# Kernel tuning notes

Hardware: AMD Instinct MI355X
Metric: run time of the kernel (lower is better)

## Reference

```python
import jax, jax.numpy as jnp
import numpy as np

EPS = 1e-5
MIN_NORM = 1e-10

def _norm(x):
    return jnp.sqrt(jnp.clip(jnp.sum(x * x, axis=-1, keepdims=True), MIN_NORM, None))

def _proj(x):
    # clip points to the open unit Poincare ball
    n = _norm(x)
    max_n = 1.0 - EPS
    return jnp.where(n > max_n, x * (max_n / n), x)

def _artanh(x):
    return jnp.arctanh(jnp.clip(x, -1.0 + EPS, 1.0 - EPS))

def mob_add(u, v):
    uv = jnp.sum(u * v, axis=-1, keepdims=True)
    u2 = jnp.sum(u * u, axis=-1, keepdims=True)
    v2 = jnp.sum(v * v, axis=-1, keepdims=True)
    num = (1.0 + 2.0 * uv + v2) * u + (1.0 - u2) * v
    den = 1.0 + 2.0 * uv + u2 * v2
    return _proj(num / jnp.maximum(den, MIN_NORM))

def mob_mat_mul(M, x):
    # M: [Din, Dout], x: [B, Din] on the ball. Ganea Mobius matvec.
    x = _proj(x)
    Mx = x @ M
    x_n = _norm(x)
    Mx_n = _norm(Mx)
    return _proj(jnp.tanh(Mx_n / x_n * _artanh(x_n)) * (Mx / Mx_n))

def log_map_zero(y):
    n = _norm(y)
    return _artanh(n) * y / n

def exp_map_zero(v):
    n = _norm(v)
    return _proj(jnp.tanh(n) * v / n)

def mob_pointwise_prod(x, u):
    # coordinate-wise scale of hyperbolic x by gate u, in the tangent space at 0
    return exp_map_zero(log_map_zero(x) * u)

def _transition(W, h, U, x, b):
    Wh = mob_mat_mul(W, h)
    Ux = mob_mat_mul(U, x)
    return mob_add(mob_add(Wh, Ux), b)

def setup_inputs() -> dict:
    B, I, H = 2048, 1024, 1024
    Din, Dh = 2 * I, 2 * H
    k = (1.0 / H) ** 0.5
    key = jax.random.key(0)
    ks = jax.random.split(key, 8)
    return {
        "hyp_x": jax.random.normal(ks[0], (B, Din), jnp.float32) * 0.01,
        "hidden": jax.random.normal(ks[1], (B, Dh), jnp.float32) * 0.01,
        "w_z": jax.random.uniform(ks[2], (Dh, Dh), jnp.float32, -k, k),
        "w_r": jax.random.uniform(ks[3], (Dh, Dh), jnp.float32, -k, k),
        "w_h": jax.random.uniform(ks[4], (Dh, Dh), jnp.float32, -k, k),
        "u_z": jax.random.uniform(ks[5], (Din, Dh), jnp.float32, -k, k),
        "u_r": jax.random.uniform(ks[6], (Din, Dh), jnp.float32, -k, k),
        "b_z": jnp.zeros((Dh,), jnp.float32),
        "b_r": jnp.zeros((Dh,), jnp.float32),
        "b_h": jnp.zeros((Dh,), jnp.float32),
    }

def reference(hyp_x, hidden, w_z, w_r, w_h, u_z, u_r, b_z, b_r, b_h):
    hyp_x = _proj(hyp_x)
    hidden = _proj(hidden)
    z = jax.nn.sigmoid(log_map_zero(_transition(w_z, hidden, u_z, hyp_x, b_z)))
    r = jax.nn.sigmoid(log_map_zero(_transition(w_r, hidden, u_r, hyp_x, b_r)))
    r_point_h = mob_pointwise_prod(hidden, r)
    # NOTE: original source uses u_r (not u_h) here; replicated faithfully.
    h_tilde = _transition(w_h, r_point_h, u_r, hyp_x, b_h)
    minus_h_oplus_htilde = mob_add(-hidden, h_tilde)
    new_h = mob_add(hidden, mob_pointwise_prod(minus_h_oplus_htilde, z))
    return new_h
```

## Files before the change

### kernel.cpp

```cpp
#include <hip/hip_runtime.h>
#include <hip/hip_bf16.h>
#include <math.h>

#define EPS 1e-5f
#define MAXN (1.0f - EPS)
#define MINN 1e-10f

constexpr int D = 2048;

typedef unsigned short u16;
typedef __bf16 bf16x8 __attribute__((ext_vector_type(8)));
typedef float floatx4 __attribute__((ext_vector_type(4)));


__device__ __forceinline__ u16 f2bf(float f) {
    union { float f; unsigned u; } v; v.f = f;
    unsigned r = v.u + 0x7FFFu + ((v.u >> 16) & 1u);
    return (u16)(r >> 16);
}

__device__ __forceinline__ float bf2f(u16 b) {
    union { unsigned u; float f; } v; v.u = ((unsigned)b) << 16; return v.f;
}

__device__ __forceinline__ void load_bf8(const u16* p, float* d) {
    uint4 r = *(const uint4*)p;
    unsigned w[4] = {r.x, r.y, r.z, r.w};
    #pragma unroll
    for (int i = 0; i < 4; ++i) {
        d[2 * i]     = bf2f((u16)(w[i] & 0xFFFFu));
        d[2 * i + 1] = bf2f((u16)(w[i] >> 16));
    }
}

__device__ __forceinline__ void store_bf8(u16* p, const float* s) {
    u16 pk[8];
    #pragma unroll
    for (int i = 0; i < 8; ++i) pk[i] = f2bf(s[i]);
    *(uint4*)p = *(const uint4*)pk;
}

__device__ __forceinline__ void load_f8(const float* p, float* d) {
    *(float4*)(d)     = *(const float4*)(p);
    *(float4*)(d + 4) = *(const float4*)(p + 4);
}

__device__ __forceinline__ void store_f8(float* p, const float* s) {
    *(float4*)(p)     = *(const float4*)(s);
    *(float4*)(p + 4) = *(const float4*)(s + 4);
}

__device__ __forceinline__ float artanh_(float x) {
    x = fminf(fmaxf(x, -1.0f + EPS), 1.0f - EPS);
    return 0.5f * logf((1.0f + x) / (1.0f - x));
}

__device__ __forceinline__ float sigmoid_(float x) {
    return 1.0f / (1.0f + expf(-x));
}

__device__ __forceinline__ void gl_lds16(const u16* g, u16* l) {
    __builtin_amdgcn_global_load_lds(
        (const __attribute__((address_space(1))) unsigned int*)g,
        (__attribute__((address_space(3))) unsigned int*)l, 16, 0, 0);
}

template<int N>
__device__ __forceinline__ void block_sums(float* v, float* sbuf) {
    #pragma unroll
    for (int n = 0; n < N; ++n)
        #pragma unroll
        for (int off = 32; off >= 1; off >>= 1) v[n] += __shfl_xor(v[n], off, 64);
    int w = threadIdx.x >> 6;
    __syncthreads();
    if ((threadIdx.x & 63) == 0) {
        #pragma unroll
        for (int n = 0; n < N; ++n) sbuf[w * N + n] = v[n];
    }
    __syncthreads();
    #pragma unroll
    for (int n = 0; n < N; ++n)
        v[n] = sbuf[n] + sbuf[N + n] + sbuf[2 * N + n] + sbuf[3 * N + n];
}

__device__ __forceinline__ void mmm_finish(float sum2, float g, float* coef, float* onorm) {
    float mxn = sqrtf(fmaxf(sum2, MINN));
    float tt  = tanhf(mxn * g);
    float on  = fminf(tt, MAXN);
    *coef = on / mxn;
    *onorm = on;
}

__device__ __forceinline__ float mob_apply(float* u, const float* v,
                                           float u2, float v2, float duv) {
    float cu  = 1.f + 2.f * duv + v2;
    float cv  = 1.f - u2;
    float den = fmaxf(1.f + 2.f * duv + u2 * v2, MINN);
    float s2  = cu * cu * u2 + 2.f * cu * cv * duv + cv * cv * v2;
    float n   = sqrtf(fmaxf(s2 / (den * den), MINN));
    float sc  = ((n > MAXN) ? MAXN / n : 1.f) / den;
    #pragma unroll
    for (int i = 0; i < 8; ++i) u[i] = sc * (cu * u[i] + cv * v[i]);
    return fminf(n, MAXN);
}

__device__ __forceinline__ void trans_tile(const float* W, u16* Wt,
                                           int n0, int k0, float* tile) {
    int t = threadIdx.x;
    int lr = t >> 4, lc = (t & 15) * 4;
    #pragma unroll
    for (int p = 0; p < 4; ++p) {
        int r = lr + p * 16;
        float4 v = *(const float4*)(W + (size_t)(k0 + r) * D + n0 + lc);
        tile[r * 65 + lc + 0] = v.x;
        tile[r * 65 + lc + 1] = v.y;
        tile[r * 65 + lc + 2] = v.z;
        tile[r * 65 + lc + 3] = v.w;
    }
    __syncthreads();
    int wn = t >> 3, ws = (t & 7) * 8;
    #pragma unroll
    for (int p = 0; p < 2; ++p) {
        int n = wn + p * 32;
        u16 pk[8];
        #pragma unroll
        for (int j = 0; j < 8; ++j) pk[j] = f2bf(tile[(ws + j) * 65 + n]);
        *(uint4*)(Wt + (size_t)(n0 + n) * D + k0 + ws) = *(uint4*)pk;
    }
}


struct PrepBatch {
    const float* W[5]; u16* Wt[5];
    const float* hx; const float* h;
    u16* hx_bf; u16* h_bf;
    float* g_x; float* g_h;
};

__global__ __launch_bounds__(256) void wtrans_prep(PrepBatch pb) {
    __shared__ float tile[64 * 65];
    int t = threadIdx.x;

    if (blockIdx.z != 4) {
        int wi = (blockIdx.z == 5) ? 4 : blockIdx.z;
        trans_tile(pb.W[wi], pb.Wt[wi],
                   blockIdx.x * 64, blockIdx.y * 64, tile);
    } else {
        int bid = blockIdx.y * (D / 64) + blockIdx.x;
        for (int rr = 0; rr < 2; ++rr) {
            int b = bid * 2 + rr;
            size_t off = (size_t)b * D + t * 8;
            float xv[8], hv[8];
            load_f8(pb.hx + off, xv);
            load_f8(pb.h + off, hv);
            float s[2] = {0.f, 0.f};
            #pragma unroll
            for (int i = 0; i < 8; ++i) { s[0] += xv[i] * xv[i]; s[1] += hv[i] * hv[i]; }
            block_sums<2>(s, tile);

            float nx = sqrtf(fmaxf(s[0], MINN));
            float scx = (nx > MAXN) ? MAXN / nx : 1.0f;
            float nh = sqrtf(fmaxf(s[1], MINN));
            float sch = (nh > MAXN) ? MAXN / nh : 1.0f;
            #pragma unroll
            for (int i = 0; i < 8; ++i) { xv[i] *= scx; hv[i] *= sch; }
            store_bf8(pb.hx_bf + off, xv);
            store_bf8(pb.h_bf + off, hv);
            if (t == 0) {
                float xn = fminf(nx, MAXN), hn = fminf(nh, MAXN);
                pb.g_x[b] = artanh_(xn) / xn;
                pb.g_h[b] = artanh_(hn) / hn;
            }
        }
    }
}


#define PHASE_MID() do { \
    __builtin_amdgcn_s_barrier(); \
    __builtin_amdgcn_s_setprio(1); } while (0)

#define PHASE_END() do { \
    __builtin_amdgcn_s_setprio(0); \
    __builtin_amdgcn_s_barrier(); } while (0)

template<int KLEN, int NJ>
__device__ __forceinline__ void gemm256_body(const u16* __restrict__ A,
                                             const u16* __restrict__ W,
                                             u16* __restrict__ C, int koff,
                                             u16* As, u16* Ws) {
    constexpr int T  = KLEN / 64;
    constexpr int BN = NJ * 64;
    constexpr int AU = 8192;
    constexpr int BU = BN * 32;

    int t0 = threadIdx.x;
    int wave = t0 >> 6, lane = t0 & 63, l16 = lane & 15, quad = lane >> 4;
    int wr = wave >> 2, wc = wave & 3;
    int brow = blockIdx.y * 256, bcol = blockIdx.x * BN;

    int srow = t0 >> 2;
    int sseg = (t0 & 3) ^ ((srow >> 1) & 3);
    const u16* srcA = A + (size_t)(brow + srow) * D + koff + sseg * 8;
    const u16* srcB = W + (size_t)(bcol + srow) * D + koff + sseg * 8;
    u16* ldsA = As + wave * 512;
    u16* ldsB = Ws + wave * 512;

    auto stageA = [&](int buf, int kh, int tile) {
        const u16* s = srcA + tile * 64 + kh * 32;
        u16* d = ldsA + (buf * 2 + kh) * AU;
        gl_lds16(s, d);
        gl_lds16(s + (size_t)128 * D, d + 4096);
    };
    auto stageB = [&](int buf, int kh, int tile) {
        const u16* s = srcB + tile * 64 + kh * 32;
        u16* d = ldsB + (buf * 2 + kh) * BU;
        gl_lds16(s, d);
        if constexpr (NJ == 4) gl_lds16(s + (size_t)128 * D, d + 4096);
    };

    const u16* aF = As + (wr * 128 + l16) * 32 + ((quad ^ ((l16 >> 1) & 3)) * 8);
    const u16* bF = Ws + (wc * (NJ * 16) + l16) * 32 + ((quad ^ ((l16 >> 1) & 3)) * 8);

    floatx4 acc[8][NJ];
    #pragma unroll
    for (int i = 0; i < 8; ++i)
        #pragma unroll
        for (int j = 0; j < NJ; ++j)
            #pragma unroll
            for (int e = 0; e < 4; ++e) acc[i][j][e] = 0.f;

    stageA(0, 0, 0); stageB(0, 0, 0);
    stageA(0, 1, 0); stageB(0, 1, 0);
    stageA(1, 0, 1); stageB(1, 0, 1);
    if constexpr (NJ == 4) asm volatile("s_waitcnt vmcnt(4)" ::: "memory");
    else                   asm volatile("s_waitcnt vmcnt(3)" ::: "memory");
    __builtin_amdgcn_s_barrier();

    #pragma unroll 2
    for (int tt = 0; tt < T; ++tt) {
        int bsel = tt & 1, bno = bsel ^ 1;
        const u16* aT = aF + bsel * (2 * AU);
        const u16* bT = bF + bsel * (2 * BU);
        bool st1 = (tt + 1) < T, st2 = (tt + 2) < T;

        if constexpr (NJ == 4) {
            bf16x8 bfr[4], afr[4];
            #pragma unroll
            for (int j = 0; j < 4; ++j) bfr[j] = *(const bf16x8*)(bT + j * 512);
            #pragma unroll
            for (int i = 0; i < 4; ++i) afr[i] = *(const bf16x8*)(aT + i * 512);
            if (st1) stageA(bno, 1, tt + 1);
            PHASE_MID();
            #pragma unroll
            for (int i = 0; i < 4; ++i)
                #pragma unroll
                for (int j = 0; j < 4; ++j)
                    acc[i][j] = __builtin_amdgcn_mfma_f32_16x16x32_bf16(afr[i], bfr[j], acc[i][j], 0, 0, 0);
            PHASE_END();
            #pragma unroll
            for (int i = 0; i < 4; ++i) afr[i] = *(const bf16x8*)(aT + (4 + i) * 512);
            if (st1) stageB(bno, 1, tt + 1);
            PHASE_MID();
            #pragma unroll
            for (int i = 0; i < 4; ++i)
                #pragma unroll
                for (int j = 0; j < 4; ++j)
                    acc[4 + i][j] = __builtin_amdgcn_mfma_f32_16x16x32_bf16(afr[i], bfr[j], acc[4 + i][j], 0, 0, 0);
            PHASE_END();
            #pragma unroll
            for (int j = 0; j < 4; ++j) bfr[j] = *(const bf16x8*)(bT + BU + j * 512);
            #pragma unroll
            for (int i = 0; i < 4; ++i) afr[i] = *(const bf16x8*)(aT + AU + i * 512);
            if (st2) stageA(bsel, 0, tt + 2);
            PHASE_MID();
            #pragma unroll
            for (int i = 0; i < 4; ++i)
                #pragma unroll
                for (int j = 0; j < 4; ++j)
                    acc[i][j] = __builtin_amdgcn_mfma_f32_16x16x32_bf16(afr[i], bfr[j], acc[i][j], 0, 0, 0);
            PHASE_END();
            #pragma unroll
            for (int i = 0; i < 4; ++i) afr[i] = *(const bf16x8*)(aT + AU + (4 + i) * 512);
            if (st2) stageB(bsel, 0, tt + 2);
            PHASE_MID();
            #pragma unroll
            for (int i = 0; i < 4; ++i)
                #pragma unroll
                for (int j = 0; j < 4; ++j)
                    acc[4 + i][j] = __builtin_amdgcn_mfma_f32_16x16x32_bf16(afr[i], bfr[j], acc[4 + i][j], 0, 0, 0);
            __builtin_amdgcn_s_setprio(0);
            asm volatile("s_waitcnt vmcnt(4)" ::: "memory");
            __builtin_amdgcn_s_barrier();
        } else {
            bf16x8 bfr[2], afr[8];
            #pragma unroll
            for (int j = 0; j < 2; ++j) bfr[j] = *(const bf16x8*)(bT + j * 512);
            #pragma unroll
            for (int i = 0; i < 8; ++i) afr[i] = *(const bf16x8*)(aT + i * 512);
            if (st1) { stageA(bno, 1, tt + 1); stageB(bno, 1, tt + 1); }
            PHASE_MID();
            #pragma unroll
            for (int i = 0; i < 8; ++i)
                #pragma unroll
                for (int j = 0; j < 2; ++j)
                    acc[i][j] = __builtin_amdgcn_mfma_f32_16x16x32_bf16(afr[i], bfr[j], acc[i][j], 0, 0, 0);
            PHASE_END();
            #pragma unroll
            for (int j = 0; j < 2; ++j) bfr[j] = *(const bf16x8*)(bT + BU + j * 512);
            #pragma unroll
            for (int i = 0; i < 8; ++i) afr[i] = *(const bf16x8*)(aT + AU + i * 512);
            if (st2) { stageA(bsel, 0, tt + 2); stageB(bsel, 0, tt + 2); }
            PHASE_MID();
            #pragma unroll
            for (int i = 0; i < 8; ++i)
                #pragma unroll
                for (int j = 0; j < 2; ++j)
                    acc[i][j] = __builtin_amdgcn_mfma_f32_16x16x32_bf16(afr[i], bfr[j], acc[i][j], 0, 0, 0);
            __builtin_amdgcn_s_setprio(0);
            asm volatile("s_waitcnt vmcnt(3)" ::: "memory");
            __builtin_amdgcn_s_barrier();
        }
    }

    #pragma unroll
    for (int i = 0; i < 8; ++i) {
        #pragma unroll
        for (int j = 0; j < NJ; ++j) {
            int row = brow + wr * 128 + i * 16 + quad * 4;
            int col = bcol + wc * (NJ * 16) + j * 16 + l16;
            #pragma unroll
            for (int r = 0; r < 4; ++r)
                C[(size_t)(row + r) * D + col] = f2bf(acc[i][j][r]);
        }
    }
}


struct G1Batch { const u16* A[4]; const u16* W[4]; u16* C[4]; };

__global__ __launch_bounds__(512, 2) void g1_kernel(G1Batch gb) {
    __shared__ u16 As[32768];
    __shared__ u16 Ws[32768];
    int z = blockIdx.z;
    gemm256_body<2048, 4>(gb.A[z], gb.W[z], gb.C[z], 0, As, Ws);
}


struct GemmBatch { const u16* A[2]; const u16* W[2]; u16* C[2]; int koff[2]; };

__global__ __launch_bounds__(512, 2) void g2_kernel(GemmBatch gb) {
    __shared__ u16 As[32768];
    __shared__ u16 Ws[16384];
    int z = blockIdx.z;
    gemm256_body<1024, 2>(gb.A[z], gb.W[z], gb.C[z], gb.koff[z], As, Ws);
}


__global__ __launch_bounds__(256) void mid_kernel(
    const u16* __restrict__ c_wz, const u16* __restrict__ c_uz,
    const u16* __restrict__ c_wr, const u16* __restrict__ c_ur,
    const u16* __restrict__ h_bf,
    const float* __restrict__ g_x, const float* __restrict__ g_h,
    const float* __restrict__ b_z, const float* __restrict__ b_r,
    u16* __restrict__ z_out, u16* __restrict__ uxr_out,
    u16* __restrict__ rph_bf, float* __restrict__ g_rph) {
    __shared__ float sbuf[24];
    int b = blockIdx.x, t = threadIdx.x;
    size_t off = (size_t)b * D + t * 8;
    int cbase = t * 8;

    float wz[8], uz[8], wr2[8], ur2[8], hp[8], bz[8], br[8];
    load_bf8(c_wz + off, wz);
    load_bf8(c_uz + off, uz);
    load_bf8(c_wr + off, wr2);
    load_bf8(c_ur + off, ur2);
    load_bf8(h_bf + off, hp);
    load_f8(b_z + cbase, bz);
    load_f8(b_r + cbase, br);

    float s[6] = {0, 0, 0, 0, 0, 0};
    #pragma unroll
    for (int i = 0; i < 8; ++i) {
        s[0] += wz[i] * wz[i];  s[1] += uz[i] * uz[i];
        s[2] += wr2[i] * wr2[i]; s[3] += ur2[i] * ur2[i];
        s[4] += bz[i] * bz[i];  s[5] += br[i] * br[i];
    }
    block_sums<6>(s, sbuf);
    float gh = g_h[b], gx = g_x[b];

    float cwz, nwz, cuz, nuz, cwr, nwr, cur, nur;
    mmm_finish(s[0], gh, &cwz, &nwz);
    mmm_finish(s[1], gx, &cuz, &nuz);
    mmm_finish(s[2], gh, &cwr, &nwr);
    mmm_finish(s[3], gx, &cur, &nur);
    #pragma unroll
    for (int i = 0; i < 8; ++i) {
        wz[i] *= cwz; uz[i] *= cuz; wr2[i] *= cwr; ur2[i] *= cur;
    }
    float sbz = s[4], sbr2 = s[5];

    float d[2] = {0.f, 0.f};
    #pragma unroll
    for (int i = 0; i < 8; ++i) { d[0] += wz[i] * uz[i]; d[1] += wr2[i] * ur2[i]; }
    block_sums<2>(d, sbuf);
    float n1z = mob_apply(wz, uz, nwz * nwz, nuz * nuz, d[0]);
    float n1r = mob_apply(wr2, ur2, nwr * nwr, nur * nur, d[1]);

    d[0] = 0.f; d[1] = 0.f;
    #pragma unroll
    for (int i = 0; i < 8; ++i) { d[0] += wz[i] * bz[i]; d[1] += wr2[i] * br[i]; }
    block_sums<2>(d, sbuf);
    float n2z = mob_apply(wz, bz, n1z * n1z, sbz, d[0]);
    float n2r = mob_apply(wr2, br, n1r * n1r, sbr2, d[1]);

    float gz = artanh_(n2z) / n2z;
    float gr = artanh_(n2r) / n2r;
    float zz[8], v[8];
    float sv = 0.f;
    #pragma unroll
    for (int i = 0; i < 8; ++i) {
        zz[i] = sigmoid_(gz * wz[i]);
        float r = sigmoid_(gr * wr2[i]);
        v[i] = gh * hp[i] * r;
        sv += v[i] * v[i];
    }
    store_bf8(z_out + off, zz);
    block_sums<1>(&sv, sbuf);
    float nv = sqrtf(fmaxf(sv, MINN));
    float th = fminf(tanhf(nv), MAXN);
    float cr = th / nv;
    #pragma unroll
    for (int i = 0; i < 8; ++i) v[i] *= cr;
    store_bf8(rph_bf + off, v);
    store_bf8(uxr_out + off, ur2);
    if (t == 0) g_rph[b] = artanh_(th) / th;
}


__global__ __launch_bounds__(256) void fin_kernel(
    const u16* __restrict__ p0, const u16* __restrict__ p1,
    const u16* __restrict__ uxr, const u16* __restrict__ z_in,
    const u16* __restrict__ h_bf,
    const float* __restrict__ g_rph, const float* __restrict__ b_h,
    float* __restrict__ out) {
    __shared__ float sbuf[16];
    int b = blockIdx.x, t = threadIdx.x;
    size_t off = (size_t)b * D + t * 8;
    int cbase = t * 8;

    float wh[8], ux[8], zz[8], hp[8], bh[8], t0[8];
    load_bf8(p0 + off, wh);
    load_bf8(p1 + off, t0);
    #pragma unroll
    for (int i = 0; i < 8; ++i) wh[i] += t0[i];
    load_bf8(uxr + off, ux);
    load_bf8(z_in + off, zz);
    load_bf8(h_bf + off, hp);
    load_f8(b_h + cbase, bh);

    float s[4] = {0, 0, 0, 0};
    #pragma unroll
    for (int i = 0; i < 8; ++i) {
        s[0] += wh[i] * wh[i]; s[1] += ux[i] * ux[i];
        s[2] += hp[i] * hp[i]; s[3] += bh[i] * bh[i];
    }
    block_sums<4>(s, sbuf);
    float swh = s[0], sux = s[1], shp = s[2], sbh = s[3];

    float cwh, nwh;
    mmm_finish(swh, g_rph[b], &cwh, &nwh);
    #pragma unroll
    for (int i = 0; i < 8; ++i) wh[i] *= cwh;

    float d = 0.f;
    #pragma unroll
    for (int i = 0; i < 8; ++i) d += wh[i] * ux[i];
    block_sums<1>(&d, sbuf);
    float n1 = mob_apply(wh, ux, nwh * nwh, sux, d);

    d = 0.f;
    #pragma unroll
    for (int i = 0; i < 8; ++i) d += wh[i] * bh[i];
    block_sums<1>(&d, sbuf);
    float nht = mob_apply(wh, bh, n1 * n1, sbh, d);

    #pragma unroll
    for (int i = 0; i < 8; ++i) ux[i] = -hp[i];
    d = 0.f;
    #pragma unroll
    for (int i = 0; i < 8; ++i) d += ux[i] * wh[i];
    block_sums<1>(&d, sbuf);
    float nm = mob_apply(ux, wh, shp, nht * nht, d);

    float lm = artanh_(nm) / nm;
    float sv = 0.f;
    #pragma unroll
    for (int i = 0; i < 8; ++i) {
        float v = lm * ux[i] * zz[i];
        ux[i] = v;
        sv += v * v;
    }
    block_sums<1>(&sv, sbuf);
    float nv = sqrtf(fmaxf(sv, MINN));
    float th = fminf(tanhf(nv), MAXN);
    float ce = th / nv;
    #pragma unroll
    for (int i = 0; i < 8; ++i) ux[i] *= ce;

    d = 0.f;
    #pragma unroll
    for (int i = 0; i < 8; ++i) d += hp[i] * ux[i];
    block_sums<1>(&d, sbuf);
    mob_apply(hp, ux, shp, th * th, d);
    store_f8(out + off, hp);
}


extern "C" void kernel_launch(void* const* d_in, const int* in_sizes, int n_in,
                              void* d_out, int out_size, void* d_ws, size_t ws_size,
                              hipStream_t stream) {
    const float* hyp_x  = (const float*)d_in[0];
    const float* hidden = (const float*)d_in[1];
    const float* w_z = (const float*)d_in[2];
    const float* w_r = (const float*)d_in[3];
    const float* w_h = (const float*)d_in[4];
    const float* u_z = (const float*)d_in[5];
    const float* u_r = (const float*)d_in[6];
    const float* b_z = (const float*)d_in[7];
    const float* b_r = (const float*)d_in[8];
    const float* b_h = (const float*)d_in[9];
    float* out = (float*)d_out;

    int B = in_sizes[1] / D;

    char* ws = (char*)d_ws;
    size_t o = 0;
    auto alloc = [&](size_t bytes) -> void* {
        void* p = ws + o;
        o += (bytes + 255) & ~(size_t)255;
        return p;
    };
    u16* wt[5];
    for (int i = 0; i < 5; ++i) wt[i] = (u16*)alloc((size_t)D * D * 2);
    u16* hx_bf = (u16*)alloc((size_t)B * D * 2);
    u16* h_bf  = (u16*)alloc((size_t)B * D * 2);
    float* g_x   = (float*)alloc((size_t)B * 4);
    float* g_h   = (float*)alloc((size_t)B * 4);
    float* g_rph = (float*)alloc((size_t)B * 4);
    u16* cz0 = (u16*)alloc((size_t)B * D * 2);
    u16* cz1 = (u16*)alloc((size_t)B * D * 2);
    u16* cz2 = (u16*)alloc((size_t)B * D * 2);
    u16* cz3 = (u16*)alloc((size_t)B * D * 2);
    u16* p0 = (u16*)alloc((size_t)B * D * 2);
    u16* p1 = (u16*)alloc((size_t)B * D * 2);
    u16* z_buf = (u16*)alloc((size_t)B * D * 2);
    u16* uxr = (u16*)alloc((size_t)B * D * 2);
    u16* rph = (u16*)alloc((size_t)B * D * 2);

    PrepBatch pb;
    pb.W[0] = w_z; pb.Wt[0] = wt[0];
    pb.W[1] = w_r; pb.Wt[1] = wt[1];
    pb.W[2] = u_z; pb.Wt[2] = wt[3];
    pb.W[3] = u_r; pb.Wt[3] = wt[4];
    pb.W[4] = w_h; pb.Wt[4] = wt[2];
    pb.hx = hyp_x; pb.h = hidden;
    pb.hx_bf = hx_bf; pb.h_bf = h_bf;
    pb.g_x = g_x; pb.g_h = g_h;
    wtrans_prep<<<dim3(D / 64, D / 64, 6), 256, 0, stream>>>(pb);

    G1Batch g1;
    g1.A[0] = h_bf;  g1.W[0] = wt[0]; g1.C[0] = cz0;
    g1.A[1] = hx_bf; g1.W[1] = wt[3]; g1.C[1] = cz1;
    g1.A[2] = h_bf;  g1.W[2] = wt[1]; g1.C[2] = cz2;
    g1.A[3] = hx_bf; g1.W[3] = wt[4]; g1.C[3] = cz3;
    g1_kernel<<<dim3(D / 256, B / 256, 4), 512, 0, stream>>>(g1);

    mid_kernel<<<dim3(B), 256, 0, stream>>>(cz0, cz1, cz2, cz3, h_bf, g_x, g_h,
                                            b_z, b_r, z_buf, uxr, rph, g_rph);

    GemmBatch g2;
    g2.A[0] = rph; g2.W[0] = wt[2]; g2.C[0] = p0; g2.koff[0] = 0;
    g2.A[1] = rph; g2.W[1] = wt[2]; g2.C[1] = p1; g2.koff[1] = 1024;
    g2_kernel<<<dim3(D / 128, B / 256, 2), 512, 0, stream>>>(g2);

    fin_kernel<<<dim3(B), 256, 0, stream>>>(p0, p1, uxr, z_buf, h_bf,
                                            g_rph, b_h, out);
}
```

Baseline: 303.9 us.

## Replace 256-row GEMM tiles with 128x128 tiles using 4-wave blocks

Both GEMM kernels switch from 256-row tiles with 8 waves to 128x128 tiles with 4 waves. Each wave now computes a 64x64 sub-tile with a simpler two-phase inner loop, and shared memory per block is halved. This gives more blocks (g1 goes from 256 to 1024 blocks) and better occupancy. In exchange, data reuse per loaded byte is lower, so global and LDS traffic rise.

```diff
diff --git a/kernel.cpp b/kernel.cpp
--- a/kernel.cpp
+++ b/kernel.cpp
@@ -184,20 +184,18 @@
     __builtin_amdgcn_s_setprio(0); \
     __builtin_amdgcn_s_barrier(); } while (0)
 
-template<int KLEN, int NJ>
-__device__ __forceinline__ void gemm256_body(const u16* __restrict__ A,
+template<int KLEN>
+__device__ __forceinline__ void gemm128_body(const u16* __restrict__ A,
                                              const u16* __restrict__ W,
                                              u16* __restrict__ C, int koff,
                                              u16* As, u16* Ws) {
     constexpr int T  = KLEN / 64;
-    constexpr int BN = NJ * 64;
-    constexpr int AU = 8192;
-    constexpr int BU = BN * 32;
+    constexpr int U  = 4096;
 
     int t0 = threadIdx.x;
     int wave = t0 >> 6, lane = t0 & 63, l16 = lane & 15, quad = lane >> 4;
-    int wr = wave >> 2, wc = wave & 3;
-    int brow = blockIdx.y * 256, bcol = blockIdx.x * BN;
+    int wr = wave >> 1, wc = wave & 1;
+    int brow = blockIdx.y * 128, bcol = blockIdx.x * 128;
 
     int srow = t0 >> 2;
     int sseg = (t0 & 3) ^ ((srow >> 1) & 3);
@@ -208,127 +206,78 @@
 
     auto stageA = [&](int buf, int kh, int tile) {
         const u16* s = srcA + tile * 64 + kh * 32;
-        u16* d = ldsA + (buf * 2 + kh) * AU;
+        u16* d = ldsA + (buf * 2 + kh) * U;
         gl_lds16(s, d);
-        gl_lds16(s + (size_t)128 * D, d + 4096);
+        gl_lds16(s + (size_t)64 * D, d + 2048);
     };
     auto stageB = [&](int buf, int kh, int tile) {
         const u16* s = srcB + tile * 64 + kh * 32;
-        u16* d = ldsB + (buf * 2 + kh) * BU;
+        u16* d = ldsB + (buf * 2 + kh) * U;
         gl_lds16(s, d);
-        if constexpr (NJ == 4) gl_lds16(s + (size_t)128 * D, d + 4096);
+        gl_lds16(s + (size_t)64 * D, d + 2048);
     };
 
-    const u16* aF = As + (wr * 128 + l16) * 32 + ((quad ^ ((l16 >> 1) & 3)) * 8);
-    const u16* bF = Ws + (wc * (NJ * 16) + l16) * 32 + ((quad ^ ((l16 >> 1) & 3)) * 8);
-
-    floatx4 acc[8][NJ];
-    #pragma unroll
-    for (int i = 0; i < 8; ++i)
-        #pragma unroll
-        for (int j = 0; j < NJ; ++j)
+    const u16* aF = As + (wr * 64 + l16) * 32 + ((quad ^ ((l16 >> 1) & 3)) * 8);
+    const u16* bF = Ws + (wc * 64 + l16) * 32 + ((quad ^ ((l16 >> 1) & 3)) * 8);
+
+    floatx4 acc[4][4];
+    #pragma unroll
+    for (int i = 0; i < 4; ++i)
+        #pragma unroll
+        for (int j = 0; j < 4; ++j)
             #pragma unroll
             for (int e = 0; e < 4; ++e) acc[i][j][e] = 0.f;
 
     stageA(0, 0, 0); stageB(0, 0, 0);
     stageA(0, 1, 0); stageB(0, 1, 0);
     stageA(1, 0, 1); stageB(1, 0, 1);
-    if constexpr (NJ == 4) asm volatile("s_waitcnt vmcnt(4)" ::: "memory");
-    else                   asm volatile("s_waitcnt vmcnt(3)" ::: "memory");
+    asm volatile("s_waitcnt vmcnt(4)" ::: "memory");
     __builtin_amdgcn_s_barrier();
 
     #pragma unroll 2
     for (int tt = 0; tt < T; ++tt) {
         int bsel = tt & 1, bno = bsel ^ 1;
-        const u16* aT = aF + bsel * (2 * AU);
-        const u16* bT = bF + bsel * (2 * BU);
+        const u16* a0 = aF + (bsel * 2 + 0) * U;
+        const u16* a1 = aF + (bsel * 2 + 1) * U;
+        const u16* b0 = bF + (bsel * 2 + 0) * U;
+        const u16* b1 = bF + (bsel * 2 + 1) * U;
         bool st1 = (tt + 1) < T, st2 = (tt + 2) < T;
 
-        if constexpr (NJ == 4) {
-            bf16x8 bfr[4], afr[4];
+        bf16x8 af[4], bf4[4];
+        #pragma unroll
+        for (int i = 0; i < 4; ++i) af[i]  = *(const bf16x8*)(a0 + i * 512);
+        #pragma unroll
+        for (int j = 0; j < 4; ++j) bf4[j] = *(const bf16x8*)(b0 + j * 512);
+        if (st1) { stageA(bno, 1, tt + 1); stageB(bno, 1, tt + 1); }
+        PHASE_MID();
+        #pragma unroll
+        for (int i = 0; i < 4; ++i)
             #pragma unroll
-            for (int j = 0; j < 4; ++j) bfr[j] = *(const bf16x8*)(bT + j * 512);
+            for (int j = 0; j < 4; ++j)
+                acc[i][j] = __builtin_amdgcn_mfma_f32_16x16x32_bf16(af[i], bf4[j], acc[i][j], 0, 0, 0);
+        PHASE_END();
+        #pragma unroll
+        for (int i = 0; i < 4; ++i) af[i]  = *(const bf16x8*)(a1 + i * 512);
+        #pragma unroll
+        for (int j = 0; j < 4; ++j) bf4[j] = *(const bf16x8*)(b1 + j * 512);
+        if (st2) { stageA(bsel, 0, tt + 2); stageB(bsel, 0, tt + 2); }
+        PHASE_MID();
+        #pragma unroll
+        for (int i = 0; i < 4; ++i)
             #pragma unroll
-            for (int i = 0; i < 4; ++i) afr[i] = *(const bf16x8*)(aT + i * 512);
-            if (st1) stageA(bno, 1, tt + 1);
-            PHASE_MID();
-            #pragma unroll
-            for (int i = 0; i < 4; ++i)
-                #pragma unroll
-                for (int j = 0; j < 4; ++j)
-                    acc[i][j] = __builtin_amdgcn_mfma_f32_16x16x32_bf16(afr[i], bfr[j], acc[i][j], 0, 0, 0);
-            PHASE_END();
-            #pragma unroll
-            for (int i = 0; i < 4; ++i) afr[i] = *(const bf16x8*)(aT + (4 + i) * 512);
-            if (st1) stageB(bno, 1, tt + 1);
-            PHASE_MID();
-            #pragma unroll
-            for (int i = 0; i < 4; ++i)
-                #pragma unroll
-                for (int j = 0; j < 4; ++j)
-                    acc[4 + i][j] = __builtin_amdgcn_mfma_f32_16x16x32_bf16(afr[i], bfr[j], acc[4 + i][j], 0, 0, 0);
-            PHASE_END();
-            #pragma unroll
-            for (int j = 0; j < 4; ++j) bfr[j] = *(const bf16x8*)(bT + BU + j * 512);
-            #pragma unroll
-            for (int i = 0; i < 4; ++i) afr[i] = *(const bf16x8*)(aT + AU + i * 512);
-            if (st2) stageA(bsel, 0, tt + 2);
-            PHASE_MID();
-            #pragma unroll
-            for (int i = 0; i < 4; ++i)
-                #pragma unroll
-                for (int j = 0; j < 4; ++j)
-                    acc[i][j] = __builtin_amdgcn_mfma_f32_16x16x32_bf16(afr[i], bfr[j], acc[i][j], 0, 0, 0);
-            PHASE_END();
-            #pragma unroll
-            for (int i = 0; i < 4; ++i) afr[i] = *(const bf16x8*)(aT + AU + (4 + i) * 512);
-            if (st2) stageB(bsel, 0, tt + 2);
-            PHASE_MID();
-            #pragma unroll
-            for (int i = 0; i < 4; ++i)
-                #pragma unroll
-                for (int j = 0; j < 4; ++j)
-                    acc[4 + i][j] = __builtin_amdgcn_mfma_f32_16x16x32_bf16(afr[i], bfr[j], acc[4 + i][j], 0, 0, 0);
-            __builtin_amdgcn_s_setprio(0);
-            asm volatile("s_waitcnt vmcnt(4)" ::: "memory");
-            __builtin_amdgcn_s_barrier();
-        } else {
-            bf16x8 bfr[2], afr[8];
-            #pragma unroll
-            for (int j = 0; j < 2; ++j) bfr[j] = *(const bf16x8*)(bT + j * 512);
-            #pragma unroll
-            for (int i = 0; i < 8; ++i) afr[i] = *(const bf16x8*)(aT + i * 512);
-            if (st1) { stageA(bno, 1, tt + 1); stageB(bno, 1, tt + 1); }
-            PHASE_MID();
-            #pragma unroll
-            for (int i = 0; i < 8; ++i)
-                #pragma unroll
-                for (int j = 0; j < 2; ++j)
-                    acc[i][j] = __builtin_amdgcn_mfma_f32_16x16x32_bf16(afr[i], bfr[j], acc[i][j], 0, 0, 0);
-            PHASE_END();
-            #pragma unroll
-            for (int j = 0; j < 2; ++j) bfr[j] = *(const bf16x8*)(bT + BU + j * 512);
-            #pragma unroll
-            for (int i = 0; i < 8; ++i) afr[i] = *(const bf16x8*)(aT + AU + i * 512);
-            if (st2) { stageA(bsel, 0, tt + 2); stageB(bsel, 0, tt + 2); }
-            PHASE_MID();
-            #pragma unroll
-            for (int i = 0; i < 8; ++i)
-                #pragma unroll
-                for (int j = 0; j < 2; ++j)
-                    acc[i][j] = __builtin_amdgcn_mfma_f32_16x16x32_bf16(afr[i], bfr[j], acc[i][j], 0, 0, 0);
-            __builtin_amdgcn_s_setprio(0);
-            asm volatile("s_waitcnt vmcnt(3)" ::: "memory");
-            __builtin_amdgcn_s_barrier();
-        }
-    }
-
-    #pragma unroll
-    for (int i = 0; i < 8; ++i) {
-        #pragma unroll
-        for (int j = 0; j < NJ; ++j) {
-            int row = brow + wr * 128 + i * 16 + quad * 4;
-            int col = bcol + wc * (NJ * 16) + j * 16 + l16;
+            for (int j = 0; j < 4; ++j)
+                acc[i][j] = __builtin_amdgcn_mfma_f32_16x16x32_bf16(af[i], bf4[j], acc[i][j], 0, 0, 0);
+        __builtin_amdgcn_s_setprio(0);
+        asm volatile("s_waitcnt vmcnt(4)" ::: "memory");
+        __builtin_amdgcn_s_barrier();
+    }
+
+    #pragma unroll
+    for (int i = 0; i < 4; ++i) {
+        #pragma unroll
+        for (int j = 0; j < 4; ++j) {
+            int row = brow + wr * 64 + i * 16 + quad * 4;
+            int col = bcol + wc * 64 + j * 16 + l16;
             #pragma unroll
             for (int r = 0; r < 4; ++r)
                 C[(size_t)(row + r) * D + col] = f2bf(acc[i][j][r]);
@@ -339,21 +288,21 @@
 
 struct G1Batch { const u16* A[4]; const u16* W[4]; u16* C[4]; };
 
-__global__ __launch_bounds__(512, 2) void g1_kernel(G1Batch gb) {
-    __shared__ u16 As[32768];
-    __shared__ u16 Ws[32768];
-    int z = blockIdx.z;
-    gemm256_body<2048, 4>(gb.A[z], gb.W[z], gb.C[z], 0, As, Ws);
-}
-
-
-struct GemmBatch { const u16* A[2]; const u16* W[2]; u16* C[2]; int koff[2]; };
-
-__global__ __launch_bounds__(512, 2) void g2_kernel(GemmBatch gb) {
-    __shared__ u16 As[32768];
+__global__ __launch_bounds__(256, 2) void g1_kernel(G1Batch gb) {
+    __shared__ u16 As[16384];
     __shared__ u16 Ws[16384];
     int z = blockIdx.z;
-    gemm256_body<1024, 2>(gb.A[z], gb.W[z], gb.C[z], gb.koff[z], As, Ws);
+    gemm128_body<2048>(gb.A[z], gb.W[z], gb.C[z], 0, As, Ws);
+}
+
+
+struct GemmBatch { const u16* A[2]; const u16* W[2]; u16* C[2]; int koff[2]; };
+
+__global__ __launch_bounds__(256, 2) void g2_kernel(GemmBatch gb) {
+    __shared__ u16 As[16384];
+    __shared__ u16 Ws[16384];
+    int z = blockIdx.z;
+    gemm128_body<1024>(gb.A[z], gb.W[z], gb.C[z], gb.koff[z], As, Ws);
 }
 
 
@@ -574,7 +523,7 @@
     g1.A[1] = hx_bf; g1.W[1] = wt[3]; g1.C[1] = cz1;
     g1.A[2] = h_bf;  g1.W[2] = wt[1]; g1.C[2] = cz2;
     g1.A[3] = hx_bf; g1.W[3] = wt[4]; g1.C[3] = cz3;
-    g1_kernel<<<dim3(D / 256, B / 256, 4), 512, 0, stream>>>(g1);
+    g1_kernel<<<dim3(D / 128, B / 128, 4), 256, 0, stream>>>(g1);
 
     mid_kernel<<<dim3(B), 256, 0, stream>>>(cz0, cz1, cz2, cz3, h_bf, g_x, g_h,
                                             b_z, b_r, z_buf, uxr, rph, g_rph);
@@ -582,7 +531,7 @@
     GemmBatch g2;
     g2.A[0] = rph; g2.W[0] = wt[2]; g2.C[0] = p0; g2.koff[0] = 0;
     g2.A[1] = rph; g2.W[1] = wt[2]; g2.C[1] = p1; g2.koff[1] = 1024;
-    g2_kernel<<<dim3(D / 128, B / 256, 2), 512, 0, stream>>>(g2);
+    g2_kernel<<<dim3(D / 128, B / 128, 2), 256, 0, stream>>>(g2);
 
     fin_kernel<<<dim3(B), 256, 0, stream>>>(p0, p1, uxr, z_buf, h_bf,
                                             g_rph, b_h, out);
```

Result: no change. 309.5 us (+1.8%).
